# Performance work log

Measured on AMD Instinct MI355X. Metric: run time of the kernel, lower is better.

## Reference

```python
import jax, jax.numpy as jnp
import numpy as np

D = 1024       # embedding_dim
H = 4096       # mlp_dim
E = 64         # num_experts
K = 3          # top-k
B, S = 2, 2048
C = 512


def setup_inputs() -> dict:
    key = jax.random.key(0)
    ks = jax.random.split(key, 6)
    s = 0.02
    return {
        "x": jax.random.normal(ks[0], (B, S, D), jnp.float32),
        "gate_w": jax.random.normal(ks[1], (D, E), jnp.float32) * s,
        "gate_b": jnp.zeros((E,), jnp.float32),
        "w1": jax.random.normal(ks[2], (E, D, H), jnp.float32) * s,
        "b1": jnp.zeros((E, H), jnp.float32),
        "w2": jax.random.normal(ks[3], (E, H, D), jnp.float32) * s,
        "b2": jnp.zeros((E, D), jnp.float32),
    }


def reference(x, gate_w, gate_b, w1, b1, w2, b2):
    xf = x.reshape(-1, D)                       # [T, D] flattened tokens
    T = xf.shape[0]
    # --- top-k gating (eval mode: clean logits, no noise) ---
    logits = xf @ gate_w + gate_b               # [T, E]
    top_l, top_i = jax.lax.top_k(logits, K)     # [T, K]
    gates = jax.nn.softmax(top_l, axis=-1)      # softmax over the k selected logits
    # --- token permutation / dispatch (capacity-based, order-preserving) ---
    fe = top_i.reshape(-1)                      # [T*K] expert id per assignment
    fg = gates.reshape(-1)                      # [T*K] gate per assignment
    tok = jnp.repeat(jnp.arange(T), K)          # [T*K] source token id
    oh = jax.nn.one_hot(fe, E, dtype=jnp.int32) # [T*K, E]
    pos = (jnp.cumsum(oh, axis=0) * oh).sum(-1) - 1  # slot within expert buffer
    valid = pos < C                             # capacity mask (C sized so nothing drops in practice)
    # scatter tokens into per-expert buffers; OOB (pos>=C) rows dropped
    buf = jnp.zeros((E, C, D), x.dtype).at[fe, pos].set(xf[tok], mode='drop')
    # --- grouped expert MLP: Linear -> exact GELU -> Linear ---
    h = jax.nn.gelu(jnp.einsum('ecd,edh->ech', buf, w1) + b1[:, None, :], approximate=False)
    y = jnp.einsum('ech,ehd->ecd', h, w2) + b2[:, None, :]  # [E, C, D]
    # --- gather back, gate, scatter-add combine ---
    rows = y[fe, jnp.minimum(pos, C - 1)] * (fg * valid.astype(x.dtype))[:, None]
    out = jnp.zeros_like(xf).at[tok].add(rows)
    return out.reshape(x.shape)
```

## Files before the change

kernel.cpp:

```cpp
#include <hip/hip_runtime.h>

#define TTOK 4096
#define DDIM 1024
#define HDIM 4096
#define NEXP 64
#define CAP  512
#define NASN (TTOK*3)

typedef unsigned short u16;
typedef __attribute__((ext_vector_type(8))) short s16x8;
typedef __attribute__((ext_vector_type(4))) short s16x4;
typedef __attribute__((ext_vector_type(4))) float f32x4;

__device__ __forceinline__ u16 f2bf(float f) {
  union { float f; unsigned u; } v; v.f = f;
  unsigned u = v.u;
  return (u16)((u + 0x7fffu + ((u >> 16) & 1u)) >> 16);
}

__device__ __forceinline__ void gl_lds16(const void* g, void* l) {
  __builtin_amdgcn_global_load_lds(
      (const __attribute__((address_space(1))) void*)g,
      (__attribute__((address_space(3))) void*)l, 16, 0, 0);
}

__global__ __launch_bounds__(256) void zero_out(float4* __restrict__ p, int n4) {
  int i = blockIdx.x * 256 + threadIdx.x;
  int st = gridDim.x * 256;
  for (; i < n4; i += st) p[i] = (float4){0.f, 0.f, 0.f, 0.f};
}

__global__ __launch_bounds__(512) void gate_topk(
    const float* __restrict__ x, const float* __restrict__ gw,
    const float* __restrict__ gb, int* __restrict__ fe, float* __restrict__ fg)
{
  int lane = threadIdx.x & 63;
  int wid  = threadIdx.x >> 6;
  int t = blockIdx.x * 8 + wid;
  const float* xr = x + (size_t)t * DDIM;
  float acc = gb[lane];
  #pragma unroll 4
  for (int d = 0; d < DDIM; d++) acc += xr[d] * gw[d * NEXP + lane];

  float v = acc;
  float bv[3]; int bi[3];
  #pragma unroll
  for (int j = 0; j < 3; j++) {
    float mv = v; int mi = lane;
    #pragma unroll
    for (int off = 32; off; off >>= 1) {
      float ov = __shfl_xor(mv, off);
      int   oi = __shfl_xor(mi, off);
      if (ov > mv || (ov == mv && oi < mi)) { mv = ov; mi = oi; }
    }
    bv[j] = mv; bi[j] = mi;
    if (lane == mi) v = -3.4e38f;
  }
  if (lane == 0) {
    float e1 = expf(bv[1] - bv[0]), e2 = expf(bv[2] - bv[0]);
    float inv = 1.0f / (1.0f + e1 + e2);
    fe[t*3+0] = bi[0]; fe[t*3+1] = bi[1]; fe[t*3+2] = bi[2];
    fg[t*3+0] = inv;   fg[t*3+1] = e1*inv; fg[t*3+2] = e2*inv;
  }
}

__global__ __launch_bounds__(64) void scan_pos(
    const int* __restrict__ fe, int* __restrict__ posA,
    int* __restrict__ s2a, int* __restrict__ cnt)
{
  int e = blockIdx.x, lane = threadIdx.x;
  int base = 0;
  for (int i0 = 0; i0 < NASN; i0 += 64) {
    int i = i0 + lane;
    bool m = (fe[i] == e);
    unsigned long long bal = __ballot(m);
    int below = __popcll(bal & ((1ull << lane) - 1ull));
    if (m) {
      int p = base + below;
      posA[i] = p;
      if (p < CAP) s2a[e * CAP + p] = i;
    }
    base += __popcll(bal);
  }
  if (lane == 0) cnt[e] = base < CAP ? base : CAP;
}

__global__ __launch_bounds__(64) void dispatch(
    const float* __restrict__ x, const int* __restrict__ fe,
    const int* __restrict__ posA, u16* __restrict__ bufA)
{
  int a = blockIdx.x;
  int p = posA[a];
  if (p >= CAP) return;
  int e = fe[a];
  int tok = a / 3;
  int l = threadIdx.x;
  const float4* xr = (const float4*)(x + (size_t)tok * DDIM);
  u16* dst = bufA + ((size_t)e * CAP + p) * DDIM;
  #pragma unroll
  for (int j = 0; j < 4; j++) {
    float4 v = xr[j * 64 + l];
    uint2 u;
    u.x = (unsigned)f2bf(v.x) | ((unsigned)f2bf(v.y) << 16);
    u.y = (unsigned)f2bf(v.z) | ((unsigned)f2bf(v.w) << 16);
    *(uint2*)(dst + (size_t)(j * 64 + l) * 4) = u;
  }
}

template<int KTOT, int NTOT, int EPI>
__global__ __launch_bounds__(256, 2) void moe_gemm(
    const u16* __restrict__ Abuf, const float* __restrict__ W,
    const float* __restrict__ bias, u16* __restrict__ hout,
    float* __restrict__ out, const int* __restrict__ cnt,
    const int* __restrict__ s2a, const float* __restrict__ fg, int g0)
{
  constexpr int NCT = NTOT / 128;
  int NB = gridDim.x;
  int b = blockIdx.x;
  int L = (b & 7) * (NB >> 3) + (b >> 3);
  int tcol = L % NCT;
  int rt   = (L / NCT) & 1;
  int el   = L / (NCT * 2);
  int e    = g0 + el;
  int cnte = cnt[e];
  int c0   = rt * 256;
  if (c0 >= cnte) return;
  int n0 = tcol * 128;

  int tid = threadIdx.x, l = tid & 63, w = tid >> 6;

  __shared__ char AsB[256 * 128];
  __shared__ char BsB[128 * 136];

  const u16* Arows = Abuf + ((size_t)((EPI == 1 ? e : el)) * CAP + c0) * (size_t)KTOT;
  const float* We = W + (size_t)e * KTOT * NTOT;

  f32x4 acc[4][8];
  #pragma unroll
  for (int m = 0; m < 4; m++)
    #pragma unroll
    for (int nn = 0; nn < 8; nn++)
      acc[m][nn] = (f32x4){0.f, 0.f, 0.f, 0.f};

  for (int k0 = 0; k0 < KTOT; k0 += 64) {
    #pragma unroll
    for (int i = 0; i < 8; i++) {
      int r = i * 32 + w * 8 + (l >> 3);
      int cswz = (l & 7) ^ (r & 7);
      const char* gsrc = (const char*)(Arows + (size_t)r * KTOT + k0) + cswz * 16;
      char* ldst = AsB + (i * 32 + w * 8) * 128;
      gl_lds16(gsrc, ldst);
    }
    {
      int n = tid & 127, kg = tid >> 7;
      #pragma unroll
      for (int j = 0; j < 8; j++) {
        int k = kg * 32 + j * 4;
        const float* p = We + (size_t)(k0 + k) * NTOT + (n0 + n);
        float v0 = p[0], v1 = p[NTOT], v2 = p[2 * NTOT], v3 = p[3 * NTOT];
        uint2 u;
        u.x = (unsigned)f2bf(v0) | ((unsigned)f2bf(v1) << 16);
        u.y = (unsigned)f2bf(v2) | ((unsigned)f2bf(v3) << 16);
        *(uint2*)(BsB + n * 136 + k * 2) = u;
      }
    }
    __syncthreads();
    #pragma unroll
    for (int k2 = 0; k2 < 2; k2++) {
      int kb = k2 * 32;
      s16x8 af[4], bf8[8];
      #pragma unroll
      for (int m = 0; m < 4; m++) {
        int R = w * 64 + m * 16 + (l & 15);
        int chunk = (kb >> 3) + (l >> 4);
        int sc = chunk ^ (R & 7);
        af[m] = *(const s16x8*)(AsB + R * 128 + sc * 16);
      }
      #pragma unroll
      for (int nn = 0; nn < 8; nn++) {
        int Nn = nn * 16 + (l & 15);
        int kk = kb + (l >> 4) * 8;
        const char* bp = BsB + Nn * 136 + kk * 2;
        union { s16x8 v8; s16x4 v4[2]; } bu;
        bu.v4[0] = *(const s16x4*)bp;
        bu.v4[1] = *(const s16x4*)(bp + 8);
        bf8[nn] = bu.v8;
      }
      #pragma unroll
      for (int m = 0; m < 4; m++)
        #pragma unroll
        for (int nn = 0; nn < 8; nn++)
          acc[m][nn] = __builtin_amdgcn_mfma_f32_16x16x32_bf16(af[m], bf8[nn], acc[m][nn], 0, 0, 0);
    }
    __syncthreads();
  }

  int lr = l >> 4, lc = l & 15;
  float bv[8];
  #pragma unroll
  for (int nn = 0; nn < 8; nn++) bv[nn] = bias[(size_t)e * NTOT + n0 + nn * 16 + lc];

  if (EPI == 1) {
    #pragma unroll
    for (int m = 0; m < 4; m++)
      #pragma unroll
      for (int nn = 0; nn < 8; nn++)
        #pragma unroll
        for (int q = 0; q < 4; q++) {
          int rowL = w * 64 + m * 16 + lr * 4 + q;
          float vv = acc[m][nn][q] + bv[nn];
          vv = 0.5f * vv * (1.0f + erff(vv * 0.70710678118f));
          hout[(size_t)(el * CAP + c0 + rowL) * NTOT + (n0 + nn * 16 + lc)] = f2bf(vv);
        }
  } else {
    #pragma unroll
    for (int m = 0; m < 4; m++) {
      int rowbase = w * 64 + m * 16 + lr * 4;
      #pragma unroll
      for (int q = 0; q < 4; q++) {
        int slot = c0 + rowbase + q;
        if (slot < cnte) {
          int aidx = s2a[e * CAP + slot];
          int tok = aidx / 3;
          float gg = fg[aidx];
          #pragma unroll
          for (int nn = 0; nn < 8; nn++) {
            float vv = (acc[m][nn][q] + bv[nn]) * gg;
            atomicAdd(out + (size_t)tok * DDIM + (n0 + nn * 16 + lc), vv);
          }
        }
      }
    }
  }
}

extern "C" void kernel_launch(void* const* d_in, const int* in_sizes, int n_in,
                              void* d_out, int out_size, void* d_ws, size_t ws_size,
                              hipStream_t stream) {
  (void)in_sizes; (void)n_in; (void)ws_size;
  const float* x  = (const float*)d_in[0];
  const float* gw = (const float*)d_in[1];
  const float* gb = (const float*)d_in[2];
  const float* w1 = (const float*)d_in[3];
  const float* b1 = (const float*)d_in[4];
  const float* w2 = (const float*)d_in[5];
  const float* b2 = (const float*)d_in[6];
  float* out = (float*)d_out;

  char* ws = (char*)d_ws;
  int*   fe   = (int*)(ws);
  float* fg   = (float*)(ws + 49152);
  int*   posA = (int*)(ws + 98304);
  int*   s2a  = (int*)(ws + 147456);
  int*   cnt  = (int*)(ws + 278528);
  u16*   bufA = (u16*)(ws + (1 << 20));
  u16*   hbuf = (u16*)(ws + (1 << 20) + 67108864ull);

  zero_out<<<1024, 256, 0, stream>>>((float4*)out, out_size / 4);
  gate_topk<<<TTOK / 8, 512, 0, stream>>>(x, gw, gb, fe, fg);
  scan_pos<<<NEXP, 64, 0, stream>>>(fe, posA, s2a, cnt);
  dispatch<<<NASN, 64, 0, stream>>>(x, fe, posA, bufA);

  moe_gemm<DDIM, HDIM, 1><<<NEXP * 2 * (HDIM / 128), 256, 0, stream>>>(
      bufA, w1, b1, hbuf, nullptr, cnt, nullptr, nullptr, 0);
  moe_gemm<HDIM, DDIM, 2><<<NEXP * 2 * (DDIM / 128), 256, 0, stream>>>(
      hbuf, w2, b2, nullptr, out, cnt, s2a, fg, 0);
}
```

Baseline: 758.5 us.

## Prefetch next weight tile into registers while computing current tile in MoE GEMM

Loads of the fp32 weight tile for the next K step are issued into a 32-register staging array before the MFMA work of the current step. Explicit waitcnt and barrier sequencing replaces __syncthreads so global weight latency overlaps compute. The GEMM1 epilogue also skips GELU and stores for rows beyond the expert's token count. This raises register pressure under launch_bounds(256,2) and relies on hand-tuned vmcnt values being correct.

Measured after the change: 742.4 us. 2.1% less time.

```diff
diff --git a/kernel.cpp b/kernel.cpp
--- a/kernel.cpp
+++ b/kernel.cpp
@@ -115,6 +115,7 @@
     const int* __restrict__ s2a, const float* __restrict__ fg, int g0)
 {
   constexpr int NCT = NTOT / 128;
+  constexpr int NT  = KTOT / 64;
   int NB = gridDim.x;
   int b = blockIdx.x;
   int L = (b & 7) * (NB >> 3) + (b >> 3);
@@ -135,6 +136,28 @@
   const u16* Arows = Abuf + ((size_t)((EPI == 1 ? e : el)) * CAP + c0) * (size_t)KTOT;
   const float* We = W + (size_t)e * KTOT * NTOT;
 
+  int bn = tid & 127, bkg = tid >> 7;
+  const float* Wt = We + (size_t)(bkg * 32) * NTOT + n0 + bn;
+  char* BsW = BsB + bn * 136 + bkg * 64;
+
+  float brB[32];
+  #define LOADB(t) { \
+    const float* p_ = Wt + (size_t)(t) * 64 * NTOT; \
+    _Pragma("unroll") \
+    for (int j_ = 0; j_ < 8; j_++) { \
+      _Pragma("unroll") \
+      for (int r_ = 0; r_ < 4; r_++) \
+        brB[j_ * 4 + r_] = p_[(size_t)(j_ * 4 + r_) * NTOT]; \
+    } }
+  #define STOREB() { \
+    _Pragma("unroll") \
+    for (int j_ = 0; j_ < 8; j_++) { \
+      uint2 u_; \
+      u_.x = (unsigned)f2bf(brB[j_*4+0]) | ((unsigned)f2bf(brB[j_*4+1]) << 16); \
+      u_.y = (unsigned)f2bf(brB[j_*4+2]) | ((unsigned)f2bf(brB[j_*4+3]) << 16); \
+      *(uint2*)(BsW + j_ * 8) = u_; \
+    } }
+
   f32x4 acc[4][8];
   #pragma unroll
   for (int m = 0; m < 4; m++)
@@ -142,29 +165,30 @@
     for (int nn = 0; nn < 8; nn++)
       acc[m][nn] = (f32x4){0.f, 0.f, 0.f, 0.f};
 
-  for (int k0 = 0; k0 < KTOT; k0 += 64) {
+  LOADB(0);
+
+  for (int t = 0; t < NT; ++t) {
     #pragma unroll
     for (int i = 0; i < 8; i++) {
       int r = i * 32 + w * 8 + (l >> 3);
       int cswz = (l & 7) ^ (r & 7);
-      const char* gsrc = (const char*)(Arows + (size_t)r * KTOT + k0) + cswz * 16;
-      char* ldst = AsB + (i * 32 + w * 8) * 128;
-      gl_lds16(gsrc, ldst);
-    }
-    {
-      int n = tid & 127, kg = tid >> 7;
-      #pragma unroll
-      for (int j = 0; j < 8; j++) {
-        int k = kg * 32 + j * 4;
-        const float* p = We + (size_t)(k0 + k) * NTOT + (n0 + n);
-        float v0 = p[0], v1 = p[NTOT], v2 = p[2 * NTOT], v3 = p[3 * NTOT];
-        uint2 u;
-        u.x = (unsigned)f2bf(v0) | ((unsigned)f2bf(v1) << 16);
-        u.y = (unsigned)f2bf(v2) | ((unsigned)f2bf(v3) << 16);
-        *(uint2*)(BsB + n * 136 + k * 2) = u;
-      }
-    }
-    __syncthreads();
+      const char* gsrc = (const char*)(Arows + (size_t)r * KTOT + (size_t)t * 64) + cswz * 16;
+      gl_lds16(gsrc, AsB + (i * 32 + w * 8) * 128);
+    }
+    STOREB();
+    __builtin_amdgcn_sched_barrier(0);
+    if (t + 1 < NT) {
+      LOADB(t + 1);
+      __builtin_amdgcn_sched_barrier(0);
+      asm volatile("s_waitcnt vmcnt(32)" ::: "memory");
+    } else {
+      asm volatile("s_waitcnt vmcnt(0)" ::: "memory");
+    }
+    asm volatile("s_waitcnt lgkmcnt(0)" ::: "memory");
+    __builtin_amdgcn_sched_barrier(0);
+    __builtin_amdgcn_s_barrier();
+    __builtin_amdgcn_sched_barrier(0);
+
     #pragma unroll
     for (int k2 = 0; k2 < 2; k2++) {
       int kb = k2 * 32;
@@ -192,7 +216,8 @@
         for (int nn = 0; nn < 8; nn++)
           acc[m][nn] = __builtin_amdgcn_mfma_f32_16x16x32_bf16(af[m], bf8[nn], acc[m][nn], 0, 0, 0);
     }
-    __syncthreads();
+    __builtin_amdgcn_s_barrier();
+    __builtin_amdgcn_sched_barrier(0);
   }
 
   int lr = l >> 4, lc = l & 15;
@@ -204,14 +229,17 @@
     #pragma unroll
     for (int m = 0; m < 4; m++)
       #pragma unroll
-      for (int nn = 0; nn < 8; nn++)
-        #pragma unroll
-        for (int q = 0; q < 4; q++) {
-          int rowL = w * 64 + m * 16 + lr * 4 + q;
-          float vv = acc[m][nn][q] + bv[nn];
-          vv = 0.5f * vv * (1.0f + erff(vv * 0.70710678118f));
-          hout[(size_t)(el * CAP + c0 + rowL) * NTOT + (n0 + nn * 16 + lc)] = f2bf(vv);
+      for (int q = 0; q < 4; q++) {
+        int rowL = w * 64 + m * 16 + lr * 4 + q;
+        if (c0 + rowL < cnte) {
+          #pragma unroll
+          for (int nn = 0; nn < 8; nn++) {
+            float vv = acc[m][nn][q] + bv[nn];
+            vv = 0.5f * vv * (1.0f + erff(vv * 0.70710678118f));
+            hout[(size_t)(el * CAP + c0 + rowL) * NTOT + (n0 + nn * 16 + lc)] = f2bf(vv);
+          }
         }
+      }
   } else {
     #pragma unroll
     for (int m = 0; m < 4; m++) {
```
